# Performance work log

Measured on AMD Instinct MI355X. Metric: run time of the kernel, lower is better.

The kernel has to match this reference:

```python
import jax, jax.numpy as jnp
import numpy as np

N, K, HC, NH, VD, NAA, AC, L = 8192, 30, 64, 8, 8, 20, 91, 4
EPS = 1e-7

def _normalize(v):
    return v / jnp.sqrt(jnp.sum(v * v, -1, keepdims=True) + EPS)

def _dihedrals(bb):
    # bb [N,4,3]; chain of N,Ca,C atoms -> phi/psi/omega -> cos/sin features [N,6]
    X = bb[:, :3].reshape(-1, 3)
    U = _normalize(X[1:] - X[:-1])
    u2, u1, u0 = U[:-2], U[1:-1], U[2:]
    n2 = _normalize(jnp.cross(u2, u1))
    n1 = _normalize(jnp.cross(u1, u0))
    cosD = jnp.clip(jnp.sum(n2 * n1, -1), -1 + EPS, 1 - EPS)
    D = jnp.sign(jnp.sum(u2 * n1, -1)) * jnp.arccos(cosD)
    D = jnp.pad(D, (1, 2)).reshape(-1, 3)
    return jnp.concatenate([jnp.cos(D), jnp.sin(D)], -1)

def _orientations(X):
    f = jnp.pad(_normalize(X[1:] - X[:-1]), ((0, 1), (0, 0)))
    b = jnp.pad(_normalize(X[:-1] - X[1:]), ((1, 0), (0, 0)))
    return jnp.stack([f, b], -2)  # [N,2,3]

def _virtual_cb(bb):
    # ideal virtual C-beta relative to Ca
    b = bb[:, 1] - bb[:, 0]
    c = bb[:, 2] - bb[:, 1]
    a = jnp.cross(b, c)
    return -0.58273431 * a + 0.56802827 * b - 0.54067466 * c

def _rbf(d, d_count=16, d_max=20.0):
    mu = jnp.linspace(0.0, d_max, d_count)
    sigma = d_max / d_count
    return jnp.exp(-(((d[..., None] - mu) / sigma) ** 2))

def _pos_emb(src, num_emb=16):
    d = (src - jnp.arange(src.shape[0])[:, None]).astype(jnp.float32)
    freq = jnp.exp(jnp.arange(0, num_emb, 2, dtype=jnp.float32) * (-np.log(10000.0) / num_emb))
    ang = d[..., None] * freq
    return jnp.concatenate([jnp.cos(ang), jnp.sin(ang)], -1)

def _edge_rot_mat(vec):
    # rotation taking world frame -> edge-aligned frame (rows x,y,z)
    z = _normalize(vec)
    ex = jnp.array([1.0, 0.0, 0.0]); ey = jnp.array([0.0, 1.0, 0.0])
    ref = jnp.where(jnp.abs(z[..., :1]) < 0.9, ex, ey)
    x = _normalize(ref - jnp.sum(ref * z, -1, keepdims=True) * z)
    y = jnp.cross(z, x)
    return jnp.stack([x, y, z], -2)

def _knn(X):
    d2 = jnp.sum((X[:, None, :] - X[None, :, :]) ** 2, -1)  # [N,N]
    i = jnp.arange(X.shape[0])
    d2 = d2.at[i, i].set(jnp.inf)
    return jax.lax.top_k(-d2, K)[1]  # [N,K] source (neighbor) ids per target

def _so3_conv(x, ef, src, R, Wrad, brad, Wgate, W0, W1):
    # equivariant edge conv: gather, rotate l=1 into edge frame, channel-mix,
    # gate by radial MLP of edge features, rotate back, aggregate over K neighbors
    xs = x[src]                                              # [N,K,4,Cin]
    s1 = jnp.einsum('nkij,nkjc->nkic', R, xs[:, :, 1:4])
    m0 = xs[:, :, 0] @ W0
    m1 = jnp.einsum('nkic,co->nkio', s1, W1)
    g0, g1 = jnp.split(jax.nn.silu(ef @ Wrad + brad) @ Wgate, 2, -1)
    m1 = jnp.einsum('nkji,nkjc->nkic', R, m1 * g1[:, :, None, :])
    return jnp.concatenate([jnp.sum(m0 * g0, 1)[:, None], jnp.sum(m1, 1)], 1) / np.sqrt(K)

def _attn(x, ef, src, R, Walpha, Wv0, Wv1, Wo):
    # SO2/SO3 graph attention: invariant alpha over K neighbors, equivariant values
    x0 = x[:, 0]
    feat = jnp.concatenate([x0[src], jnp.broadcast_to(x0[:, None], (N, K, x0.shape[-1])), ef], -1)
    a = jax.nn.softmax(jax.nn.leaky_relu(feat @ Walpha, 0.2), axis=1)  # [N,K,NH]
    xs = x[src]
    s1 = jnp.einsum('nkij,nkjc->nkic', R, xs[:, :, 1:4])
    v0 = (xs[:, :, 0] @ Wv0).reshape(N, K, NH, VD)
    v1 = jnp.einsum('nkic,ch->nkih', s1, Wv1).reshape(N, K, 3, NH, VD)
    o0 = jnp.sum(v0 * a[..., None], 1).reshape(N, NH * VD)
    v1 = (v1 * a[:, :, None, :, None]).reshape(N, K, 3, NH * VD)
    o1 = jnp.sum(jnp.einsum('nkji,nkjc->nkic', R, v1), 1)
    return jnp.concatenate([o0[:, None], o1], 1) @ Wo

def _ffn(x, W1, W2):
    t = x[:, 0] @ W1
    h1 = jnp.einsum('nic,ch->nih', x[:, 1:4], W1) * jax.nn.sigmoid(t)[:, None, :]
    return jnp.concatenate([(jax.nn.silu(t) @ W2)[:, None], jnp.einsum('nih,ho->nio', h1, W2)], 1)

def _forward(bb, seq, latent, eb_Wrad, eb_brad, eb_Wgate, eb_W0, eb_W1, t_Walpha, t_Wv0, t_Wv1, t_Wo, t_Wf1, t_Wf2, e_W, e_b, p_Walpha, p_Wv0, p_Wv1, p_Wo, p_Wf1, p_Wf2, oa_Wrad, oa_brad, oa_Wgate, oa_W0, oa_W1, ln_g, ln_b, W_seq, b_seq, src):
    X_ca = bb[:, 1]
    vec = X_ca[src] - X_ca[:, None]                     # [N,K,3]
    R = _edge_rot_mat(vec)
    dist = jnp.sqrt(jnp.sum(vec * vec, -1) + EPS)
    ef = jnp.concatenate([_rbf(dist), _pos_emb(src)], -1)  # [N,K,32]
    # bb SO3 embedding: l=0 -> dihedrals + seq one-hot (masked to zero per noising_mask);
    # l=1 -> 7 relative vectors (4 bb_rel, 2 orientations, 1 virtual Cb), zero-padded to 26 ch
    scal = jnp.concatenate([_dihedrals(bb), jnp.zeros((N, NAA), bb.dtype)], -1)
    vecs = jnp.nan_to_num(jnp.concatenate([bb - X_ca[:, None], _orientations(X_ca), _virtual_cb(bb)[:, None]], 1))
    l1 = jnp.zeros((N, 3, scal.shape[-1]), bb.dtype).at[:, :, :7].set(jnp.transpose(vecs, (0, 2, 1)))
    bbemb = jnp.concatenate([scal[:, None], l1], 1)     # [N,4,26]
    bbout = _so3_conv(bbemb, ef, src, R, eb_Wrad, eb_brad, eb_Wgate, eb_W0, eb_W1)  # [N,4,32]
    res = jnp.concatenate([bbout, latent], -1)          # [N,4,64]
    for i in range(L):
        res = res + _attn(res, ef, src, R, t_Walpha[i], t_Wv0[i], t_Wv1[i], t_Wo[i])
        res = res + _ffn(res, t_Wf1[i], t_Wf2[i])
        efeat = jnp.concatenate([res[:, 0][src], jnp.broadcast_to(res[:, 0][:, None], (N, K, HC)), ef], -1)
        ef = jnp.tanh(efeat @ e_W[i] + e_b[i])
    p = _attn(res, ef, src, R, p_Walpha, p_Wv0, p_Wv1, p_Wo)  # [N,4,32]
    p = p + _ffn(p, p_Wf1, p_Wf2)
    atoms = _so3_conv(p, ef, src, R, oa_Wrad, oa_brad, oa_Wgate, oa_W0, oa_W1)  # [N,4,91]
    inv = atoms[:, 0]
    mu = jnp.mean(inv, -1, keepdims=True)
    var = jnp.var(inv, -1, keepdims=True)
    logits = jax.nn.log_softmax(((inv - mu) / jnp.sqrt(var + 1e-5) * ln_g + ln_b) @ W_seq + b_seq, -1)
    decoded = jnp.transpose(atoms[:, 1:4], (0, 2, 1))   # [N,91,3]
    return decoded, logits

def setup_inputs():
    key = jax.random.key(0)
    ks = jax.random.split(key, 30)
    def p(k, shape, fan):
        return jax.random.normal(k, shape, jnp.float32) * (fan ** -0.5)
    ca = jnp.cumsum(jax.random.normal(ks[0], (N, 3)) * 2.2, 0)
    bb = ca[:, None, :] + jax.random.normal(ks[1], (N, 4, 3)) * 0.8
    CA160 = 2 * HC + 32
    return {
        'bb': bb,
        'seq': jax.random.randint(ks[2], (N,), 0, NAA),
        'latent': jax.random.normal(ks[3], (N, 4, HC // 2)),
        'eb_Wrad': p(ks[4], (32, 64), 32), 'eb_brad': jnp.zeros((64,)),
        'eb_Wgate': p(ks[5], (64, 64), 64), 'eb_W0': p(ks[6], (26, 32), 26), 'eb_W1': p(ks[7], (26, 32), 26),
        't_Walpha': p(ks[8], (L, CA160, NH), CA160),
        't_Wv0': p(ks[9], (L, HC, NH * VD), HC), 't_Wv1': p(ks[10], (L, HC, NH * VD), HC),
        't_Wo': p(ks[11], (L, NH * VD, HC), NH * VD),
        't_Wf1': p(ks[12], (L, HC, HC), HC), 't_Wf2': p(ks[13], (L, HC, HC), HC),
        'e_W': p(ks[14], (L, CA160, 32), CA160), 'e_b': jnp.zeros((L, 32)),
        'p_Walpha': p(ks[15], (CA160, NH), CA160),
        'p_Wv0': p(ks[16], (HC, NH * VD), HC), 'p_Wv1': p(ks[17], (HC, NH * VD), HC),
        'p_Wo': p(ks[18], (NH * VD, 32), NH * VD),
        'p_Wf1': p(ks[19], (32, 32), 32), 'p_Wf2': p(ks[20], (32, 32), 32),
        'oa_Wrad': p(ks[21], (32, 64), 32), 'oa_brad': jnp.zeros((64,)),
        'oa_Wgate': p(ks[22], (64, 2 * AC), 64), 'oa_W0': p(ks[23], (32, AC), 32), 'oa_W1': p(ks[24], (32, AC), 32),
        'ln_g': jnp.ones((AC,)), 'ln_b': jnp.zeros((AC,)),
        'W_seq': p(ks[25], (AC, NAA), AC), 'b_seq': jnp.zeros((NAA,)),
    }

def reference(bb, seq, latent, eb_Wrad, eb_brad, eb_Wgate, eb_W0, eb_W1, t_Walpha, t_Wv0, t_Wv1, t_Wo, t_Wf1, t_Wf2, e_W, e_b, p_Walpha, p_Wv0, p_Wv1, p_Wo, p_Wf1, p_Wf2, oa_Wrad, oa_brad, oa_Wgate, oa_W0, oa_W1, ln_g, ln_b, W_seq, b_seq):
    src = _knn(bb[:, 1])
    return _forward(bb, seq, latent, eb_Wrad, eb_brad, eb_Wgate, eb_W0, eb_W1, t_Walpha, t_Wv0, t_Wv1, t_Wo, t_Wf1, t_Wf2, e_W, e_b, p_Walpha, p_Wv0, p_Wv1, p_Wo, p_Wf1, p_Wf2, oa_Wrad, oa_brad, oa_Wgate, oa_W0, oa_W1, ln_g, ln_b, W_seq, b_seq, src)
```

## Files before the change

### kernel.cpp

```cpp
#include <hip/hip_runtime.h>
#include <math.h>


#define NN 8192
#define KK 30
#define NE (NN*KK)
#define EPSF 1e-7f

static const size_t O_SRC = 0;
static const size_t O_XS  = 1ull<<20;
static const size_t O_YS  = O_XS + (size_t)NN*4;
static const size_t O_ZS  = O_XS + (size_t)NN*8;
static const size_t O_BBE = 2ull<<20;
static const size_t O_RES = 6ull<<20;
static const size_t O_P   = 15ull<<20;
static const size_t O_EF  = 20ull<<20;
static const size_t O_NF  = 52ull<<20;
static const size_t O_V1  = 55ull<<20;
static const size_t O_O   = 62ull<<20;
static const size_t O_EE  = 71ull<<20;
static const size_t O_M0E = 52ull<<20;
static const size_t O_M1E = 54ull<<20;
static const size_t O_M0O = 52ull<<20;
static const size_t O_M1O = 56ull<<20;
static const size_t O_ATM = 6ull<<20;
static const size_t WS_NEEDED = 80ull<<20;

__device__ __forceinline__ float nn0(float v){ return (v != v) ? 0.f : v; }
__device__ __forceinline__ void norm3(float& x, float& y, float& z){
  float s = sqrtf(x*x + y*y + z*z + EPSF);
  x /= s; y /= s; z /= s;
}

__global__ void k_prep(const float* __restrict__ bb, float* __restrict__ xs,
                       float* __restrict__ ys, float* __restrict__ zs,
                       float* __restrict__ bbe){
  int n = blockIdx.x*blockDim.x + threadIdx.x;
  if (n >= NN) return;
  const float* bn = bb + (size_t)n*12;
  float a0x=bn[0],a0y=bn[1],a0z=bn[2];
  float cax=bn[3],cay=bn[4],caz=bn[5];
  float a2x=bn[6],a2y=bn[7],a2z=bn[8];
  float a3x=bn[9],a3y=bn[10],a3z=bn[11];
  xs[n]=cax; ys[n]=cay; zs[n]=caz;
  float v[7][3];
  v[0][0]=a0x-cax; v[0][1]=a0y-cay; v[0][2]=a0z-caz;
  v[1][0]=0.f;     v[1][1]=0.f;     v[1][2]=0.f;
  v[2][0]=a2x-cax; v[2][1]=a2y-cay; v[2][2]=a2z-caz;
  v[3][0]=a3x-cax; v[3][1]=a3y-cay; v[3][2]=a3z-caz;
  if (n < NN-1){
    float fx=bb[(size_t)(n+1)*12+3]-cax, fy=bb[(size_t)(n+1)*12+4]-cay, fz=bb[(size_t)(n+1)*12+5]-caz;
    norm3(fx,fy,fz); v[4][0]=fx; v[4][1]=fy; v[4][2]=fz;
  } else { v[4][0]=v[4][1]=v[4][2]=0.f; }
  if (n > 0){
    float gx=bb[(size_t)(n-1)*12+3]-cax, gy=bb[(size_t)(n-1)*12+4]-cay, gz=bb[(size_t)(n-1)*12+5]-caz;
    norm3(gx,gy,gz); v[5][0]=gx; v[5][1]=gy; v[5][2]=gz;
  } else { v[5][0]=v[5][1]=v[5][2]=0.f; }
  {
    float bx=cax-a0x, by=cay-a0y, bz=caz-a0z;
    float cx=a2x-cax, cy=a2y-cay, cz=a2z-caz;
    float ax = by*cz - bz*cy, ay = bz*cx - bx*cz, az = bx*cy - by*cx;
    v[6][0] = -0.58273431f*ax + 0.56802827f*bx - 0.54067466f*cx;
    v[6][1] = -0.58273431f*ay + 0.56802827f*by - 0.54067466f*cy;
    v[6][2] = -0.58273431f*az + 0.56802827f*bz - 0.54067466f*cz;
  }
  float* be = bbe + (size_t)n*104;
  #pragma unroll
  for (int c=6;c<26;++c) be[c]=0.f;
  #pragma unroll
  for (int s=0;s<3;++s){
    float* br = be + 26*(1+s);
    #pragma unroll
    for (int c=0;c<26;++c) br[c] = (c<7) ? nn0(v[c][s]) : 0.f;
  }
}

__global__ void k_dihed(const float* __restrict__ bb, float* __restrict__ bbe){
  int t = blockIdx.x*blockDim.x + threadIdx.x;
  if (t >= 3*NN) return;
  float cD = 1.f, sD = 0.f;
  if (t >= 1 && t < 3*NN-2){
    int i = t-1;
    float p[4][3];
    #pragma unroll
    for (int m=0;m<4;++m){
      int a = i+m; int rn = a/3, ra = a - rn*3;
      const float* q = bb + (size_t)(rn*4 + ra)*3;
      p[m][0]=q[0]; p[m][1]=q[1]; p[m][2]=q[2];
    }
    float u2x=p[1][0]-p[0][0], u2y=p[1][1]-p[0][1], u2z=p[1][2]-p[0][2];
    float u1x=p[2][0]-p[1][0], u1y=p[2][1]-p[1][1], u1z=p[2][2]-p[1][2];
    float u0x=p[3][0]-p[2][0], u0y=p[3][1]-p[2][1], u0z=p[3][2]-p[2][2];
    norm3(u2x,u2y,u2z); norm3(u1x,u1y,u1z); norm3(u0x,u0y,u0z);
    float n2x=u2y*u1z-u2z*u1y, n2y=u2z*u1x-u2x*u1z, n2z=u2x*u1y-u2y*u1x;
    float n1x=u1y*u0z-u1z*u0y, n1y=u1z*u0x-u1x*u0z, n1z=u1x*u0y-u1y*u0x;
    norm3(n2x,n2y,n2z); norm3(n1x,n1y,n1z);
    float cosD = n2x*n1x + n2y*n1y + n2z*n1z;
    const float lo = (float)(-1.0 + 1e-7), hi = (float)(1.0 - 1e-7);
    cosD = fminf(fmaxf(cosD, lo), hi);
    float sg = u2x*n1x + u2y*n1y + u2z*n1z;
    float sgn = (sg > 0.f) ? 1.f : ((sg < 0.f) ? -1.f : 0.f);
    float D = sgn * acosf(cosD);
    cD = cosf(D); sD = sinf(D);
  }
  int n = t/3, col = t - n*3;
  bbe[(size_t)n*104 + col] = cD;
  bbe[(size_t)n*104 + 3 + col] = sD;
}

__global__ __launch_bounds__(256) void k_knn(const float* __restrict__ xs,
        const float* __restrict__ ys, const float* __restrict__ zs, int* __restrict__ src){
  __shared__ float sd[4][32];
  __shared__ int   si[4][32];
  int w = threadIdx.x >> 6, lane = threadIdx.x & 63;
  int n = blockIdx.x*4 + w;
  float qx = xs[n], qy = ys[n], qz = zs[n];
  if (lane >= 30 && lane < 32){ sd[w][lane] = INFINITY; si[w][lane] = 0; }

  int w0 = n - 32; if (w0 < 0) w0 = 0; if (w0 > NN-64) w0 = NN-64;
  int idx = w0 + lane;
  {
    float dx = qx - xs[idx], dy = qy - ys[idx], dz = qz - zs[idx];
    float d2 = dx*dx + dy*dy + dz*dz;
    if (idx == n) d2 = INFINITY;
    #pragma unroll
    for (int k = 2; k <= 64; k <<= 1){
      #pragma unroll
      for (int jj = k>>1; jj >= 1; jj >>= 1){
        float od = __shfl_xor(d2, jj);
        int   oi = __shfl_xor(idx, jj);
        bool up      = ((lane & k) == 0);
        bool lower   = ((lane & jj) == 0);
        bool takeMin = (up == lower);
        bool mless   = (d2 < od) || (d2 == od && idx < oi);
        if (mless != takeMin){ d2 = od; idx = oi; }
      }
    }
    if (lane < 30){ sd[w][lane] = d2; si[w][lane] = idx; }
  }
  float thr = sd[w][29];

  for (int s = 0; s < NN/64; ++s){
    int j = s*64 + lane;
    float dx = __fsub_rn(qx, xs[j]);
    float dy = __fsub_rn(qy, ys[j]);
    float dz = __fsub_rn(qz, zs[j]);
    float d2 = __fadd_rn(__fadd_rn(__fmul_rn(dx,dx),__fmul_rn(dy,dy)),__fmul_rn(dz,dz));
    if (j == n) d2 = INFINITY;
    if (j >= w0 && j < w0+64) d2 = INFINITY;
    unsigned long long bal = __ballot(d2 < thr);
    if (bal){
      while (bal){
        int b = __ffsll((unsigned long long)bal) - 1;
        bal &= bal - 1ull;
        float vd = __shfl(d2, b);
        int vj = s*64 + b;
        float dl = 0.f; int il = 0; bool keep = true;
        if (lane < 30){ dl = sd[w][lane]; il = si[w][lane]; keep = (dl <= vd); }
        unsigned long long km = __ballot(lane < 30 && keep);
        int pos = __popcll(km);
        if (lane < 30 && !keep){ sd[w][lane+1] = dl; si[w][lane+1] = il; }
        if (lane == pos){ sd[w][lane] = vd; si[w][lane] = vj; }
      }
      thr = sd[w][29];
    }
  }
  if (lane < 30) src[(size_t)n*KK + lane] = si[w][lane];
}

__global__ void k_edgefeat(const int* __restrict__ src, const float* __restrict__ xs,
        const float* __restrict__ ys, const float* __restrict__ zs, float* __restrict__ ef){
  int e = blockIdx.x*blockDim.x + threadIdx.x;
  if (e >= NE) return;
  int n = e / KK;
  int j = src[e];
  float vx = xs[j]-xs[n], vy = ys[j]-ys[n], vz = zs[j]-zs[n];
  float dist = sqrtf(vx*vx + vy*vy + vz*vz + EPSF);
  float* o = ef + (size_t)e*32;
  #pragma unroll
  for (int m=0;m<16;++m){
    float mu = (float)m * (20.f/15.f);
    float q = (dist - mu) / 1.25f;
    o[m] = expf(-q*q);
  }
  float d = (float)(j - n);
  const float Cf = -0.5756462732485115f;
  #pragma unroll
  for (int fi=0; fi<8; ++fi){
    float fr = expf((float)(2*fi) * Cf);
    float ang = d * fr;
    o[16+fi] = cosf(ang);
    o[24+fi] = sinf(ang);
  }
}

template<int K, int ACT, int BSEL>
__global__ __launch_bounds__(256) void k_gemm(const float* __restrict__ A,
        const float* __restrict__ B1, const float* __restrict__ B2,
        const float* __restrict__ bias, float* __restrict__ C,
        int M, int Nc, int ldc, int arpg, int agst, int arst, int aoff, int beta){
  constexpr int KP = (K+3)&~3;
  constexpr int SP = ((KP+4)%32==0) ? KP+8 : KP+4;
  __shared__ alignas(16) float As[64*SP];
  __shared__ alignas(16) float Bs[KP*64];
  int tid = threadIdx.x, tm = blockIdx.x, tn = blockIdx.y;
  for (int i = tid; i < KP*64; i += 256){
    int kk = i >> 6, cl = i & 63;
    int c = tn*64 + cl;
    float v = 0.f;
    if (c < Nc && kk < K){
      if (BSEL == 0) v = B1[kk*Nc + c];
      else if (BSEL == 1) v = (c<8) ? B1[kk*8+c] : ((c<16) ? B1[(64+kk)*8 + (c-8)] : B2[kk*64 + (c-16)]);
      else v = (c<32) ? B1[kk*32 + c] : B1[(64+kk)*32 + (c-32)];
    }
    Bs[i] = v;
  }
  for (int i = tid; i < 64*KP; i += 256){
    int rl = i / KP, kk = i - rl*KP;
    int r = tm*64 + rl;
    float v = 0.f;
    if (r < M && kk < K){
      const float* ap;
      if (arpg == 1) ap = A + (size_t)r*agst + aoff;
      else { int g = r/3; int wr = r - g*3; ap = A + (size_t)g*agst + wr*arst + aoff; }
      v = ap[kk];
    }
    As[rl*SP + kk] = v;
  }
  __syncthreads();
  int tx = tid & 15, ty = tid >> 4;
  float acc[4][4] = {};
  #pragma unroll 2
  for (int kq = 0; kq < KP/4; ++kq){
    float4 a0 = *reinterpret_cast<const float4*>(&As[(ty*4+0)*SP + kq*4]);
    float4 a1 = *reinterpret_cast<const float4*>(&As[(ty*4+1)*SP + kq*4]);
    float4 a2 = *reinterpret_cast<const float4*>(&As[(ty*4+2)*SP + kq*4]);
    float4 a3 = *reinterpret_cast<const float4*>(&As[(ty*4+3)*SP + kq*4]);
    #pragma unroll
    for (int mm = 0; mm < 4; ++mm){
      float4 b4 = *reinterpret_cast<const float4*>(&Bs[(kq*4+mm)*64 + tx*4]);
      float e0 = (&a0.x)[mm], e1 = (&a1.x)[mm], e2 = (&a2.x)[mm], e3 = (&a3.x)[mm];
      acc[0][0] += e0*b4.x; acc[0][1] += e0*b4.y; acc[0][2] += e0*b4.z; acc[0][3] += e0*b4.w;
      acc[1][0] += e1*b4.x; acc[1][1] += e1*b4.y; acc[1][2] += e1*b4.z; acc[1][3] += e1*b4.w;
      acc[2][0] += e2*b4.x; acc[2][1] += e2*b4.y; acc[2][2] += e2*b4.z; acc[2][3] += e2*b4.w;
      acc[3][0] += e3*b4.x; acc[3][1] += e3*b4.y; acc[3][2] += e3*b4.z; acc[3][3] += e3*b4.w;
    }
  }
  if (ACT == 2){
    int r0 = tm*64 + ty*4;
    #pragma unroll
    for (int cc = 0; cc < 4; ++cc){
      int c = tn*64 + tx*4 + cc;
      if (c >= Nc) continue;
      float t0 = acc[0][cc];
      float g = 1.f/(1.f + expf(-t0));
      C[(size_t)(r0+0)*ldc + c] = t0*g;
      C[(size_t)(r0+1)*ldc + c] = acc[1][cc]*g;
      C[(size_t)(r0+2)*ldc + c] = acc[2][cc]*g;
      C[(size_t)(r0+3)*ldc + c] = acc[3][cc]*g;
    }
  } else {
    #pragma unroll
    for (int rr = 0; rr < 4; ++rr){
      int r = tm*64 + ty*4 + rr;
      if (r >= M) continue;
      #pragma unroll
      for (int cc = 0; cc < 4; ++cc){
        int c = tn*64 + tx*4 + cc;
        if (c >= Nc) continue;
        float v = acc[rr][cc];
        if (bias) v += bias[c];
        size_t ci = (size_t)r*ldc + c;
        if (beta) v += C[ci];
        C[ci] = v;
      }
    }
  }
}

__global__ __launch_bounds__(256) void k_attn(const int* __restrict__ src,
        const float* __restrict__ NF, const float* __restrict__ V1,
        const float* __restrict__ ef, const float* __restrict__ WaE, float* __restrict__ o){
  int w = threadIdx.x >> 6, lane = threadIdx.x & 63;
  int n = blockIdx.x*4 + w;
  int h = lane >> 3, q = lane & 7;
  float w0 = WaE[(q*4+0)*8 + h];
  float w1 = WaE[(q*4+1)*8 + h];
  float w2 = WaE[(q*4+2)*8 + h];
  float w3 = WaE[(q*4+3)*8 + h];
  const int* sk = src + (size_t)n*KK;
  int myj = (lane < KK) ? sk[lane] : 0;
  float a2 = NF[(size_t)n*80 + 8 + h];
  float m = -INFINITY, s = 0.f, o0=0.f, o1=0.f, o2=0.f, o3=0.f;
  for (int k = 0; k < KK; ++k){
    int j = __shfl(myj, k);
    float4 e4 = *reinterpret_cast<const float4*>(ef + ((size_t)n*KK + k)*32 + q*4);
    float val = e4.x*w0 + e4.y*w1 + e4.z*w2 + e4.w*w3;
    val += __shfl_xor(val, 1);
    val += __shfl_xor(val, 2);
    val += __shfl_xor(val, 4);
    float l = val + NF[(size_t)j*80 + h] + a2;
    l = (l >= 0.f) ? l : 0.2f*l;
    float mn = fmaxf(m, l);
    float f = expf(m - mn);
    float pp = expf(l - mn);
    s = s*f + pp;
    const float* v1p = V1 + (size_t)j*192;
    o0 = o0*f + pp*NF[(size_t)j*80 + 16 + lane];
    o1 = o1*f + pp*v1p[lane];
    o2 = o2*f + pp*v1p[64+lane];
    o3 = o3*f + pp*v1p[128+lane];
    m = mn;
  }
  float inv = 1.f/s;
  float* op = o + (size_t)n*256;
  op[lane] = o0*inv; op[64+lane] = o1*inv; op[128+lane] = o2*inv; op[192+lane] = o3*inv;
}

template<int C>
__global__ __launch_bounds__(256) void k_so3fused(const int* __restrict__ src,
        const float* __restrict__ ef, const float* __restrict__ Wrad,
        const float* __restrict__ brad, const float* __restrict__ Wgate,
        const float* __restrict__ M0, const float* __restrict__ M1,
        const float* __restrict__ lat, float* __restrict__ out, int nstr, int sstr){
  constexpr int KT = (C==32) ? 2 : 4;
  constexpr int KG = 32/KT;
  constexpr int NQ = (C==32) ? 16 : 23;
  constexpr int PW = (C==32) ? 32 : 92;
  constexpr int CG = (C==32) ? 64 : 92;
  constexpr int HS = 68;
  constexpr int NPASS = (C==32) ? 1 : 2;
  constexpr int NT = KG*NQ;
  constexpr int LD0 = PW;
  constexpr int LD1 = PW;
  __shared__ alignas(16) float uni[64*CG];
  __shared__ alignas(16) float Hs[32*HS];
  __shared__ alignas(16) float part[4*KG*PW];
  __shared__ int js[32];
  float* efs = uni;
  float* Wr  = uni + 30*32;
  float* Wg  = uni;
  int n = blockIdx.x, tid = threadIdx.x;
  for (int i = tid; i < KK*32; i += 256) efs[i] = ef[(size_t)n*KK*32 + i];
  for (int i = tid; i < 2048;  i += 256) Wr[i]  = Wrad[i];
  if (tid < 32) js[tid] = (tid < KK) ? src[(size_t)n*KK + tid] : 0;
  __syncthreads();
  for (int i = tid; i < 32*64; i += 256){
    int k = i >> 6, h = i & 63;
    float v = 0.f;
    if (k < KK){
      float a = brad[h];
      const float* er = efs + k*32;
      #pragma unroll
      for (int m = 0; m < 32; ++m) a += er[m]*Wr[m*64 + h];
      v = a/(1.f + expf(-a));
    }
    Hs[k*HS + h] = v;
  }
  int kg = tid / NQ, cq = tid - kg*NQ;
  bool act = (tid < NT);
  for (int pass = 0; pass < NPASS; ++pass){
    __syncthreads();
    for (int i = tid; i < 64*CG; i += 256){
      int m = i/CG, u = i - m*CG;
      float v = 0.f;
      if (C == 32) v = Wgate[m*64 + u];
      else if (u < 91) v = Wgate[m*182 + pass*91 + u];
      Wg[i] = v;
    }
    __syncthreads();
    if (act){
      float g[KT][4];
      #pragma unroll
      for (int i=0;i<KT;++i){ g[i][0]=0.f; g[i][1]=0.f; g[i][2]=0.f; g[i][3]=0.f; }
      #pragma unroll 2
      for (int mq = 0; mq < 16; ++mq){
        float4 hs[KT];
        #pragma unroll
        for (int i=0;i<KT;++i) hs[i] = *reinterpret_cast<const float4*>(&Hs[(kg*KT+i)*HS + mq*4]);
        #pragma unroll
        for (int mm=0; mm<4; ++mm){
          float4 w4 = *reinterpret_cast<const float4*>(&Wg[(mq*4+mm)*CG + cq*4]);
          #pragma unroll
          for (int i=0;i<KT;++i){
            float h = (&hs[i].x)[mm];
            g[i][0] += h*w4.x; g[i][1] += h*w4.y; g[i][2] += h*w4.z; g[i][3] += h*w4.w;
          }
        }
      }
      bool scalar_path = (C==32) ? (cq < 8) : (pass == 0);
      if (scalar_path){
        int c = cq*4;
        float a0x=0.f, a0y=0.f, a0z=0.f, a0w=0.f;
        #pragma unroll
        for (int i=0;i<KT;++i){
          int k = kg*KT+i;
          float4 m0 = *reinterpret_cast<const float4*>(&M0[(size_t)js[k]*LD0 + c]);
          a0x += g[i][0]*m0.x; a0y += g[i][1]*m0.y; a0z += g[i][2]*m0.z; a0w += g[i][3]*m0.w;
        }
        float4 r4; r4.x=a0x; r4.y=a0y; r4.z=a0z; r4.w=a0w;
        *reinterpret_cast<float4*>(&part[(0*KG+kg)*PW + c]) = r4;
      } else {
        int c = (C==32) ? (cq*4-32) : cq*4;
        float a1[4]={0,0,0,0}, a2[4]={0,0,0,0}, a3[4]={0,0,0,0};
        #pragma unroll
        for (int i=0;i<KT;++i){
          int k = kg*KT+i;
          const float* m1r = M1 + (size_t)js[k]*3*LD1;
          float4 v1 = *reinterpret_cast<const float4*>(&m1r[c]);
          float4 v2 = *reinterpret_cast<const float4*>(&m1r[LD1 + c]);
          float4 v3 = *reinterpret_cast<const float4*>(&m1r[2*LD1 + c]);
          a1[0]+=g[i][0]*v1.x; a1[1]+=g[i][1]*v1.y; a1[2]+=g[i][2]*v1.z; a1[3]+=g[i][3]*v1.w;
          a2[0]+=g[i][0]*v2.x; a2[1]+=g[i][1]*v2.y; a2[2]+=g[i][2]*v2.z; a2[3]+=g[i][3]*v2.w;
          a3[0]+=g[i][0]*v3.x; a3[1]+=g[i][1]*v3.y; a3[2]+=g[i][2]*v3.z; a3[3]+=g[i][3]*v3.w;
        }
        float4 r1; r1.x=a1[0]; r1.y=a1[1]; r1.z=a1[2]; r1.w=a1[3];
        float4 r2; r2.x=a2[0]; r2.y=a2[1]; r2.z=a2[2]; r2.w=a2[3];
        float4 r3; r3.x=a3[0]; r3.y=a3[1]; r3.z=a3[2]; r3.w=a3[3];
        *reinterpret_cast<float4*>(&part[(1*KG+kg)*PW + c]) = r1;
        *reinterpret_cast<float4*>(&part[(2*KG+kg)*PW + c]) = r2;
        *reinterpret_cast<float4*>(&part[(3*KG+kg)*PW + c]) = r3;
      }
    }
  }
  __syncthreads();
  const float IS = 0.18257418583505536f;
  for (int idx = tid; idx < 4*C; idx += 256){
    int r = idx / C, c = idx - r*C;
    float s = 0.f;
    #pragma unroll
    for (int gq = 0; gq < KG; ++gq) s += part[(r*KG+gq)*PW + c];
    out[(size_t)n*nstr + r*sstr + c] = s*IS;
  }
  if (C == 32){
    if (lat){
      for (int idx = tid; idx < 128; idx += 256){
        int r = idx >> 5, c = idx & 31;
        out[(size_t)n*nstr + r*sstr + 32 + c] = lat[(size_t)n*128 + r*32 + c];
      }
    }
  }
}

__global__ __launch_bounds__(256) void k_edgeout(const int* __restrict__ src,
        const float* __restrict__ eWe, const float* __restrict__ EE,
        const float* __restrict__ ebv, float* __restrict__ ef){
  __shared__ float ws[32*32];
  __shared__ float es[8*32];
  int tid = threadIdx.x;
  size_t e0 = (size_t)blockIdx.x*8;
  for (int i = tid; i < 1024; i += 256) ws[i] = eWe[i];
  es[tid] = ef[e0*32 + tid];
  __syncthreads();
  int le = tid >> 5, c = tid & 31;
  size_t e = e0 + le;
  int n = (int)(e / KK);
  int j = src[e];
  float acc = ebv[c] + EE[(size_t)j*64 + c] + EE[(size_t)n*64 + 32 + c];
  const float* er = es + le*32;
  #pragma unroll
  for (int kk = 0; kk < 32; ++kk) acc += er[kk]*ws[kk*32 + c];
  ef[e*32 + c] = tanhf(acc);
}

__global__ __launch_bounds__(128) void k_head(const float* __restrict__ atoms,
        const float* __restrict__ ln_g, const float* __restrict__ ln_b,
        const float* __restrict__ W_seq, const float* __restrict__ b_seq, float* __restrict__ out){
  __shared__ float red[128];
  __shared__ float nrm[91];
  __shared__ float lg[20];
  int n = blockIdx.x, t = threadIdx.x;
  const float* inv = atoms + (size_t)n*364;
  float x = (t < 91) ? inv[t] : 0.f;
  red[t] = x; __syncthreads();
  for (int off=64; off>=1; off>>=1){ if (t<off) red[t]+=red[t+off]; __syncthreads(); }
  float mu = red[0] / 91.f;
  __syncthreads();
  float d = x - mu;
  red[t] = (t<91) ? d*d : 0.f; __syncthreads();
  for (int off=64; off>=1; off>>=1){ if (t<off) red[t]+=red[t+off]; __syncthreads(); }
  float var = red[0] / 91.f;
  __syncthreads();
  if (t < 91) nrm[t] = (x - mu)/sqrtf(var + 1e-5f) * ln_g[t] + ln_b[t];
  __syncthreads();
  if (t < 20){
    float acc = b_seq[t];
    for (int c=0;c<91;++c) acc += nrm[c]*W_seq[c*20+t];
    lg[t] = acc;
  }
  __syncthreads();
  if (t == 0){
    float mx = lg[0];
    for (int i=1;i<20;++i) mx = fmaxf(mx, lg[i]);
    float s = 0.f;
    for (int i=0;i<20;++i) s += expf(lg[i]-mx);
    red[0] = mx + logf(s);
  }
  __syncthreads();
  float lse = red[0];
  if (t < 20) out[(size_t)NN*273 + (size_t)n*20 + t] = lg[t] - lse;
  for (int idx = t; idx < 273; idx += 128){
    int c = idx/3, i = idx - c*3;
    out[(size_t)n*273 + idx] = atoms[(size_t)n*364 + (1+i)*91 + c];
  }
}

static void gemm(hipStream_t st, int K, int act, int bsel, const float* A,
                 const float* B1, const float* B2, const float* bias, float* C,
                 int M, int Nc, int ldc, int arpg, int agst, int arst, int aoff, int beta){
  dim3 g((M+63)/64, (Nc+63)/64), b(256);
  if (K == 26){
    k_gemm<26,0,0><<<g,b,0,st>>>(A,B1,B2,bias,C,M,Nc,ldc,arpg,agst,arst,aoff,beta);
  } else if (K == 32){
    if (act == 2) k_gemm<32,2,0><<<g,b,0,st>>>(A,B1,B2,bias,C,M,Nc,ldc,arpg,agst,arst,aoff,beta);
    else          k_gemm<32,0,0><<<g,b,0,st>>>(A,B1,B2,bias,C,M,Nc,ldc,arpg,agst,arst,aoff,beta);
  } else {
    if (act == 2)        k_gemm<64,2,0><<<g,b,0,st>>>(A,B1,B2,bias,C,M,Nc,ldc,arpg,agst,arst,aoff,beta);
    else if (bsel == 1)  k_gemm<64,0,1><<<g,b,0,st>>>(A,B1,B2,bias,C,M,Nc,ldc,arpg,agst,arst,aoff,beta);
    else if (bsel == 2)  k_gemm<64,0,2><<<g,b,0,st>>>(A,B1,B2,bias,C,M,Nc,ldc,arpg,agst,arst,aoff,beta);
    else                 k_gemm<64,0,0><<<g,b,0,st>>>(A,B1,B2,bias,C,M,Nc,ldc,arpg,agst,arst,aoff,beta);
  }
}

extern "C" void kernel_launch(void* const* d_in, const int* in_sizes, int n_in,
                              void* d_out, int out_size, void* d_ws, size_t ws_size,
                              hipStream_t stream){
  (void)in_sizes; (void)n_in; (void)out_size;
  if (ws_size < WS_NEEDED) return;

  const float* bb      = (const float*)d_in[0];
  const float* latent  = (const float*)d_in[2];
  const float* eb_Wrad = (const float*)d_in[3];
  const float* eb_brad = (const float*)d_in[4];
  const float* eb_Wgate= (const float*)d_in[5];
  const float* eb_W0   = (const float*)d_in[6];
  const float* eb_W1   = (const float*)d_in[7];
  const float* t_Walpha= (const float*)d_in[8];
  const float* t_Wv0   = (const float*)d_in[9];
  const float* t_Wv1   = (const float*)d_in[10];
  const float* t_Wo    = (const float*)d_in[11];
  const float* t_Wf1   = (const float*)d_in[12];
  const float* t_Wf2   = (const float*)d_in[13];
  const float* e_W     = (const float*)d_in[14];
  const float* e_b     = (const float*)d_in[15];
  const float* p_Walpha= (const float*)d_in[16];
  const float* p_Wv0   = (const float*)d_in[17];
  const float* p_Wv1   = (const float*)d_in[18];
  const float* p_Wo    = (const float*)d_in[19];
  const float* p_Wf1   = (const float*)d_in[20];
  const float* p_Wf2   = (const float*)d_in[21];
  const float* oa_Wrad = (const float*)d_in[22];
  const float* oa_brad = (const float*)d_in[23];
  const float* oa_Wgate= (const float*)d_in[24];
  const float* oa_W0   = (const float*)d_in[25];
  const float* oa_W1   = (const float*)d_in[26];
  const float* ln_g    = (const float*)d_in[27];
  const float* ln_b    = (const float*)d_in[28];
  const float* W_seq   = (const float*)d_in[29];
  const float* b_seq   = (const float*)d_in[30];

  char* w = (char*)d_ws;
  int*   src = (int*)  (w + O_SRC);
  float* xs  = (float*)(w + O_XS);
  float* ys  = (float*)(w + O_YS);
  float* zs  = (float*)(w + O_ZS);
  float* bbe = (float*)(w + O_BBE);
  float* res = (float*)(w + O_RES);
  float* p   = (float*)(w + O_P);
  float* ef  = (float*)(w + O_EF);
  float* NF  = (float*)(w + O_NF);
  float* V1  = (float*)(w + O_V1);
  float* o   = (float*)(w + O_O);
  float* EE  = (float*)(w + O_EE);
  float* M0e = (float*)(w + O_M0E);
  float* M1e = (float*)(w + O_M1E);
  float* M0o = (float*)(w + O_M0O);
  float* M1o = (float*)(w + O_M1O);
  float* atm = (float*)(w + O_ATM);

  k_prep <<<(NN+255)/256, 256, 0, stream>>>(bb, xs, ys, zs, bbe);
  k_dihed<<<(3*NN+255)/256, 256, 0, stream>>>(bb, bbe);
  k_knn  <<<NN/4, 256, 0, stream>>>(xs, ys, zs, src);
  k_edgefeat<<<(NE+255)/256, 256, 0, stream>>>(src, xs, ys, zs, ef);

  gemm(stream, 26,0,0, bbe, eb_W0, nullptr, nullptr, M0e, NN,   32, 32, 1,104, 0, 0, 0);
  gemm(stream, 26,0,0, bbe, eb_W1, nullptr, nullptr, M1e, 3*NN, 32, 32, 3,104,26,26, 0);
  k_so3fused<32><<<NN, 256, 0, stream>>>(src, ef, eb_Wrad, eb_brad, eb_Wgate, M0e, M1e, latent, res, 256, 64);

  for (int L=0; L<4; ++L){
    const float* Wa  = t_Walpha + (size_t)L*160*8;
    const float* Wv0 = t_Wv0 + (size_t)L*64*64;
    const float* Wv1 = t_Wv1 + (size_t)L*64*64;
    const float* Wo  = t_Wo  + (size_t)L*64*64;
    const float* Wf1 = t_Wf1 + (size_t)L*64*64;
    const float* Wf2 = t_Wf2 + (size_t)L*64*64;
    const float* eWl = e_W   + (size_t)L*160*32;
    const float* ebl = e_b   + (size_t)L*32;
    gemm(stream, 64,0,1, res, Wa, Wv0, nullptr, NF, NN,   80, 80, 1,256, 0, 0, 0);
    gemm(stream, 64,0,0, res, Wv1, nullptr, nullptr, V1, 3*NN, 64, 64, 3,256,64,64, 0);
    k_attn<<<NN/4, 256, 0, stream>>>(src, NF, V1, ef, Wa + 128*8, o);
    gemm(stream, 64,0,0, o,   Wo,  nullptr, nullptr, res, 4*NN, 64, 64, 1,64,0,0, 1);
    gemm(stream, 64,2,0, res, Wf1, nullptr, nullptr, o,   4*NN, 64, 64, 1,64,0,0, 0);
    gemm(stream, 64,0,0, o,   Wf2, nullptr, nullptr, res, 4*NN, 64, 64, 1,64,0,0, 1);
    gemm(stream, 64,0,2, res, eWl, nullptr, nullptr, EE,  NN,   64, 64, 1,256,0,0, 0);
    k_edgeout<<<NE/8, 256, 0, stream>>>(src, eWl + 128*32, EE, ebl, ef);
  }

  gemm(stream, 64,0,1, res, p_Walpha, p_Wv0, nullptr, NF, NN,   80, 80, 1,256, 0, 0, 0);
  gemm(stream, 64,0,0, res, p_Wv1, nullptr, nullptr, V1, 3*NN, 64, 64, 3,256,64,64, 0);
  k_attn<<<NN/4, 256, 0, stream>>>(src, NF, V1, ef, p_Walpha + 128*8, o);
  gemm(stream, 64,0,0, o, p_Wo,  nullptr, nullptr, p, 4*NN, 32, 32, 1,64,0,0, 0);
  gemm(stream, 32,2,0, p, p_Wf1, nullptr, nullptr, o, 4*NN, 32, 32, 1,32,0,0, 0);
  gemm(stream, 32,0,0, o, p_Wf2, nullptr, nullptr, p, 4*NN, 32, 32, 1,32,0,0, 1);

  gemm(stream, 32,0,0, p, oa_W0, nullptr, nullptr, M0o, NN,   91, 92, 1,128, 0, 0, 0);
  gemm(stream, 32,0,0, p, oa_W1, nullptr, nullptr, M1o, 3*NN, 91, 92, 3,128,32,32, 0);
  k_so3fused<91><<<NN, 256, 0, stream>>>(src, ef, oa_Wrad, oa_brad, oa_Wgate, M0o, M1o, nullptr, atm, 364, 91);

  k_head<<<NN, 128, 0, stream>>>(atm, ln_g, ln_b, W_seq, b_seq, (float*)d_out);
}
```

Measured before the change: 1.371 ms.

## Read gate weights directly from global memory in fused SO3 conv, single pass

The per-node SO3 conv kernel no longer stages the gate weight matrix into shared memory in one or two passes. It reads float4 weights straight from global (L2-cached) memory. For the output-head case the weights are repacked once into a padded 184-wide layout so both halves (scalar and vector) are computed in one pass, with 46 column quads and 5 edge groups of 6 edges. The partial-sum buffer is padded to avoid bank conflicts. This removes per-block weight copies and barriers but adds global loads in the inner loop and changes thread utilization (230 of 256 threads active).

```diff
diff --git a/kernel.cpp b/kernel.cpp
--- a/kernel.cpp
+++ b/kernel.cpp
@@ -24,6 +24,7 @@
 static const size_t O_M0O = 52ull<<20;
 static const size_t O_M1O = 56ull<<20;
 static const size_t O_ATM = 6ull<<20;
+static const size_t O_WGO = 78ull<<20;
 static const size_t WS_NEEDED = 80ull<<20;
 
 __device__ __forceinline__ float nn0(float v){ return (v != v) ? 0.f : v; }
@@ -317,32 +318,39 @@
   op[lane] = o0*inv; op[64+lane] = o1*inv; op[128+lane] = o2*inv; op[192+lane] = o3*inv;
 }
 
+__global__ void k_wgrepack(const float* __restrict__ Wg, float* __restrict__ o){
+  int i = blockIdx.x*blockDim.x + threadIdx.x;
+  if (i >= 64*184) return;
+  int m = i/184, c = i - m*184;
+  float v = 0.f;
+  if (c < 91) v = Wg[m*182 + c];
+  else if (c >= 92 && c < 183) v = Wg[m*182 + 91 + (c - 92)];
+  o[i] = v;
+}
+
 template<int C>
 __global__ __launch_bounds__(256) void k_so3fused(const int* __restrict__ src,
         const float* __restrict__ ef, const float* __restrict__ Wrad,
-        const float* __restrict__ brad, const float* __restrict__ Wgate,
+        const float* __restrict__ brad, const float* __restrict__ Wg,
         const float* __restrict__ M0, const float* __restrict__ M1,
         const float* __restrict__ lat, float* __restrict__ out, int nstr, int sstr){
-  constexpr int KT = (C==32) ? 2 : 4;
-  constexpr int KG = 32/KT;
-  constexpr int NQ = (C==32) ? 16 : 23;
-  constexpr int PW = (C==32) ? 32 : 92;
-  constexpr int CG = (C==32) ? 64 : 92;
-  constexpr int HS = 68;
-  constexpr int NPASS = (C==32) ? 1 : 2;
-  constexpr int NT = KG*NQ;
-  constexpr int LD0 = PW;
-  constexpr int LD1 = PW;
-  __shared__ alignas(16) float uni[64*CG];
-  __shared__ alignas(16) float Hs[32*HS];
-  __shared__ alignas(16) float part[4*KG*PW];
+  constexpr int NQ   = (C==32) ? 16 : 46;
+  constexpr int KG   = (C==32) ? 16 : 5;
+  constexpr int KT   = (C==32) ? 2  : 6;
+  constexpr int WGS  = (C==32) ? 64 : 184;
+  constexpr int HALF = NQ/2;
+  constexpr int PW   = (C==32) ? 32 : 92;
+  constexpr int PWS  = (PW%32==0) ? PW+4 : PW;
+  constexpr int LD0  = PW;
+  constexpr int LD1  = PW;
+  constexpr int POOL = (2048 > 4*KG*PWS) ? 2048 : 4*KG*PWS;
+  __shared__ alignas(16) float efs[KK*32];
+  __shared__ alignas(16) float pool[POOL];
+  __shared__ alignas(16) float Hs[32*68];
   __shared__ int js[32];
-  float* efs = uni;
-  float* Wr  = uni + 30*32;
-  float* Wg  = uni;
   int n = blockIdx.x, tid = threadIdx.x;
   for (int i = tid; i < KK*32; i += 256) efs[i] = ef[(size_t)n*KK*32 + i];
-  for (int i = tid; i < 2048;  i += 256) Wr[i]  = Wrad[i];
+  for (int i = tid; i < 2048;  i += 256) pool[i] = Wrad[i];
   if (tid < 32) js[tid] = (tid < KK) ? src[(size_t)n*KK + tid] : 0;
   __syncthreads();
   for (int i = tid; i < 32*64; i += 256){
@@ -352,75 +360,64 @@
       float a = brad[h];
       const float* er = efs + k*32;
       #pragma unroll
-      for (int m = 0; m < 32; ++m) a += er[m]*Wr[m*64 + h];
+      for (int m = 0; m < 32; ++m) a += er[m]*pool[m*64 + h];
       v = a/(1.f + expf(-a));
     }
-    Hs[k*HS + h] = v;
-  }
-  int kg = tid / NQ, cq = tid - kg*NQ;
-  bool act = (tid < NT);
-  for (int pass = 0; pass < NPASS; ++pass){
-    __syncthreads();
-    for (int i = tid; i < 64*CG; i += 256){
-      int m = i/CG, u = i - m*CG;
-      float v = 0.f;
-      if (C == 32) v = Wgate[m*64 + u];
-      else if (u < 91) v = Wgate[m*182 + pass*91 + u];
-      Wg[i] = v;
-    }
-    __syncthreads();
-    if (act){
-      float g[KT][4];
+    Hs[k*68 + h] = v;
+  }
+  __syncthreads();
+  float* part = pool;
+  int kg = tid / NQ, q = tid - kg*NQ;
+  if (kg < KG){
+    float g[KT][4];
+    #pragma unroll
+    for (int i=0;i<KT;++i){ g[i][0]=0.f; g[i][1]=0.f; g[i][2]=0.f; g[i][3]=0.f; }
+    #pragma unroll 2
+    for (int mq = 0; mq < 16; ++mq){
+      float4 hs[KT];
       #pragma unroll
-      for (int i=0;i<KT;++i){ g[i][0]=0.f; g[i][1]=0.f; g[i][2]=0.f; g[i][3]=0.f; }
-      #pragma unroll 2
-      for (int mq = 0; mq < 16; ++mq){
-        float4 hs[KT];
+      for (int i=0;i<KT;++i) hs[i] = *reinterpret_cast<const float4*>(&Hs[(kg*KT+i)*68 + mq*4]);
+      #pragma unroll
+      for (int mm=0; mm<4; ++mm){
+        float4 w4 = *reinterpret_cast<const float4*>(&Wg[(mq*4+mm)*WGS + q*4]);
         #pragma unroll
-        for (int i=0;i<KT;++i) hs[i] = *reinterpret_cast<const float4*>(&Hs[(kg*KT+i)*HS + mq*4]);
-        #pragma unroll
-        for (int mm=0; mm<4; ++mm){
-          float4 w4 = *reinterpret_cast<const float4*>(&Wg[(mq*4+mm)*CG + cq*4]);
-          #pragma unroll
-          for (int i=0;i<KT;++i){
-            float h = (&hs[i].x)[mm];
-            g[i][0] += h*w4.x; g[i][1] += h*w4.y; g[i][2] += h*w4.z; g[i][3] += h*w4.w;
-          }
+        for (int i=0;i<KT;++i){
+          float h = (&hs[i].x)[mm];
+          g[i][0] += h*w4.x; g[i][1] += h*w4.y; g[i][2] += h*w4.z; g[i][3] += h*w4.w;
         }
       }
-      bool scalar_path = (C==32) ? (cq < 8) : (pass == 0);
-      if (scalar_path){
-        int c = cq*4;
-        float a0x=0.f, a0y=0.f, a0z=0.f, a0w=0.f;
-        #pragma unroll
-        for (int i=0;i<KT;++i){
-          int k = kg*KT+i;
-          float4 m0 = *reinterpret_cast<const float4*>(&M0[(size_t)js[k]*LD0 + c]);
-          a0x += g[i][0]*m0.x; a0y += g[i][1]*m0.y; a0z += g[i][2]*m0.z; a0w += g[i][3]*m0.w;
-        }
-        float4 r4; r4.x=a0x; r4.y=a0y; r4.z=a0z; r4.w=a0w;
-        *reinterpret_cast<float4*>(&part[(0*KG+kg)*PW + c]) = r4;
-      } else {
-        int c = (C==32) ? (cq*4-32) : cq*4;
-        float a1[4]={0,0,0,0}, a2[4]={0,0,0,0}, a3[4]={0,0,0,0};
-        #pragma unroll
-        for (int i=0;i<KT;++i){
-          int k = kg*KT+i;
-          const float* m1r = M1 + (size_t)js[k]*3*LD1;
-          float4 v1 = *reinterpret_cast<const float4*>(&m1r[c]);
-          float4 v2 = *reinterpret_cast<const float4*>(&m1r[LD1 + c]);
-          float4 v3 = *reinterpret_cast<const float4*>(&m1r[2*LD1 + c]);
-          a1[0]+=g[i][0]*v1.x; a1[1]+=g[i][1]*v1.y; a1[2]+=g[i][2]*v1.z; a1[3]+=g[i][3]*v1.w;
-          a2[0]+=g[i][0]*v2.x; a2[1]+=g[i][1]*v2.y; a2[2]+=g[i][2]*v2.z; a2[3]+=g[i][3]*v2.w;
-          a3[0]+=g[i][0]*v3.x; a3[1]+=g[i][1]*v3.y; a3[2]+=g[i][2]*v3.z; a3[3]+=g[i][3]*v3.w;
-        }
-        float4 r1; r1.x=a1[0]; r1.y=a1[1]; r1.z=a1[2]; r1.w=a1[3];
-        float4 r2; r2.x=a2[0]; r2.y=a2[1]; r2.z=a2[2]; r2.w=a2[3];
-        float4 r3; r3.x=a3[0]; r3.y=a3[1]; r3.z=a3[2]; r3.w=a3[3];
-        *reinterpret_cast<float4*>(&part[(1*KG+kg)*PW + c]) = r1;
-        *reinterpret_cast<float4*>(&part[(2*KG+kg)*PW + c]) = r2;
-        *reinterpret_cast<float4*>(&part[(3*KG+kg)*PW + c]) = r3;
+    }
+    if (q < HALF){
+      int c = q*4;
+      float a0[4] = {0.f,0.f,0.f,0.f};
+      #pragma unroll
+      for (int i=0;i<KT;++i){
+        int k = kg*KT+i;
+        float4 m0 = *reinterpret_cast<const float4*>(&M0[(size_t)js[k]*LD0 + c]);
+        a0[0]+=g[i][0]*m0.x; a0[1]+=g[i][1]*m0.y; a0[2]+=g[i][2]*m0.z; a0[3]+=g[i][3]*m0.w;
       }
+      float4 r0; r0.x=a0[0]; r0.y=a0[1]; r0.z=a0[2]; r0.w=a0[3];
+      *reinterpret_cast<float4*>(&part[(0*KG+kg)*PWS + c]) = r0;
+    } else {
+      int c = (q-HALF)*4;
+      float a1[4]={0.f,0.f,0.f,0.f}, a2[4]={0.f,0.f,0.f,0.f}, a3[4]={0.f,0.f,0.f,0.f};
+      #pragma unroll
+      for (int i=0;i<KT;++i){
+        int k = kg*KT+i;
+        const float* m1r = M1 + (size_t)js[k]*3*LD1;
+        float4 v1 = *reinterpret_cast<const float4*>(&m1r[c]);
+        float4 v2 = *reinterpret_cast<const float4*>(&m1r[LD1 + c]);
+        float4 v3 = *reinterpret_cast<const float4*>(&m1r[2*LD1 + c]);
+        a1[0]+=g[i][0]*v1.x; a1[1]+=g[i][1]*v1.y; a1[2]+=g[i][2]*v1.z; a1[3]+=g[i][3]*v1.w;
+        a2[0]+=g[i][0]*v2.x; a2[1]+=g[i][1]*v2.y; a2[2]+=g[i][2]*v2.z; a2[3]+=g[i][3]*v2.w;
+        a3[0]+=g[i][0]*v3.x; a3[1]+=g[i][1]*v3.y; a3[2]+=g[i][2]*v3.z; a3[3]+=g[i][3]*v3.w;
+      }
+      float4 r1; r1.x=a1[0]; r1.y=a1[1]; r1.z=a1[2]; r1.w=a1[3];
+      float4 r2; r2.x=a2[0]; r2.y=a2[1]; r2.z=a2[2]; r2.w=a2[3];
+      float4 r3; r3.x=a3[0]; r3.y=a3[1]; r3.z=a3[2]; r3.w=a3[3];
+      *reinterpret_cast<float4*>(&part[(1*KG+kg)*PWS + c]) = r1;
+      *reinterpret_cast<float4*>(&part[(2*KG+kg)*PWS + c]) = r2;
+      *reinterpret_cast<float4*>(&part[(3*KG+kg)*PWS + c]) = r3;
     }
   }
   __syncthreads();
@@ -429,7 +426,7 @@
     int r = idx / C, c = idx - r*C;
     float s = 0.f;
     #pragma unroll
-    for (int gq = 0; gq < KG; ++gq) s += part[(r*KG+gq)*PW + c];
+    for (int gq = 0; gq < KG; ++gq) s += part[(r*KG+gq)*PWS + c];
     out[(size_t)n*nstr + r*sstr + c] = s*IS;
   }
   if (C == 32){
@@ -577,6 +574,7 @@
   float* M0o = (float*)(w + O_M0O);
   float* M1o = (float*)(w + O_M1O);
   float* atm = (float*)(w + O_ATM);
+  float* Wgo = (float*)(w + O_WGO);
 
   k_prep <<<(NN+255)/256, 256, 0, stream>>>(bb, xs, ys, zs, bbe);
   k_dihed<<<(3*NN+255)/256, 256, 0, stream>>>(bb, bbe);
@@ -615,7 +613,8 @@
 
   gemm(stream, 32,0,0, p, oa_W0, nullptr, nullptr, M0o, NN,   91, 92, 1,128, 0, 0, 0);
   gemm(stream, 32,0,0, p, oa_W1, nullptr, nullptr, M1o, 3*NN, 91, 92, 3,128,32,32, 0);
-  k_so3fused<91><<<NN, 256, 0, stream>>>(src, ef, oa_Wrad, oa_brad, oa_Wgate, M0o, M1o, nullptr, atm, 364, 91);
+  k_wgrepack<<<46, 256, 0, stream>>>(oa_Wgate, Wgo);
+  k_so3fused<91><<<NN, 256, 0, stream>>>(src, ef, oa_Wrad, oa_brad, Wgo, M0o, M1o, nullptr, atm, 364, 91);
 
   k_head<<<NN, 128, 0, stream>>>(atm, ln_g, ln_b, W_seq, b_seq, (float*)d_out);
 }
```

After: 1.296 ms. -5.4%, faster.
